# Kernel optimization log

Hardware: AMD Instinct MI355X
Metric: run time of the kernel (lower is better)

The kernel has to match this reference:

```python
import jax, jax.numpy as jnp
import numpy as np

B, N, DIN, DINNER, DOUT, W = 4, 8192, 512, 512, 512, 128


def setup_inputs() -> dict:
    key = jax.random.key(0)
    k1, k2, k3 = jax.random.split(key, 3)
    x = jax.random.normal(k1, (B, N, DIN), jnp.float32)
    # torch Linear weights: (out_features, in_features)
    w_qkv = jax.random.normal(k2, (3 * DINNER, DIN), jnp.float32) * (DIN ** -0.5)
    w_out = jax.random.normal(k3, (DOUT, DINNER), jnp.float32) * (DINNER ** -0.5)
    b_out = jnp.zeros((DOUT,), jnp.float32)
    return {"x": x, "w_qkv": w_qkv, "w_out": w_out, "b_out": b_out}


def reference(x, w_qkv, w_out, b_out):
    b, n, _ = x.shape
    w = W
    scale = DINNER ** -0.5
    pad = (-n) % w  # pad_to_multiple along seq dim (static)
    xp = jnp.pad(x, ((0, 0), (0, pad), (0, 0)))
    qkv = jnp.einsum('bnd,ed->bne', xp, w_qkv)  # to_qkv, no bias
    q, k, v = jnp.split(qkv, 3, axis=-1)
    win = lambda t: t.reshape(b, -1, w, DINNER)  # b (w n) d -> b w n d
    q, k, v = win(q), win(k), win(v)
    # prepend one zero bucket to k, then overlap prev/current windows.
    kp = jnp.pad(k, ((0, 0), (1, 0), (0, 0), (0, 0)))
    k2 = jnp.concatenate((kp[:, :-1], kp[:, 1:]), axis=2)  # (b, nb, 2w, d)
    # NOTE: source bug replicated — v is also built from k, not v.
    v2 = jnp.concatenate((kp[:, :-1], kp[:, 1:]), axis=2)
    sim = jnp.einsum('bwid,bwjd->bwij', q, k2) * scale  # (b, nb, w, 2w)
    i, j = w, 2 * w
    mask = jnp.triu(jnp.ones((i, j), bool), j - i + 1)
    sim = jnp.where(mask, -jnp.finfo(sim.dtype).max, sim)
    attn = jax.nn.softmax(sim, axis=-1)
    out = jnp.einsum('bwij,bwjd->bwid', attn, v2)
    out = out.reshape(b, -1, DINNER)[:, :n]
    return jnp.einsum('bnd,od->bno', out, w_out) + b_out
```

## Files before the change

kernel.cpp:

```cpp
#include <hip/hip_runtime.h>
#include <cstdint>
#include <cstddef>

typedef float f32x4 __attribute__((ext_vector_type(4)));
typedef short s16x8 __attribute__((ext_vector_type(8)));
typedef short s16x4 __attribute__((ext_vector_type(4)));

#define MFMA_BF16(a, b, c) __builtin_amdgcn_mfma_f32_16x16x32_bf16((a), (b), (c), 0, 0, 0)

#define GLD16(g, l)                                                            \
  __builtin_amdgcn_global_load_lds(                                            \
      (const __attribute__((address_space(1))) void*)(g),                      \
      (__attribute__((address_space(3))) void*)(l), 16, 0, 0)

__device__ __forceinline__ unsigned short f2bf(float f) {
  unsigned int u = __float_as_uint(f);
  u += 0x7FFFu + ((u >> 16) & 1u);
  return (unsigned short)(u >> 16);
}

__device__ __forceinline__ s16x8 cvt8(const float* __restrict__ src) {
  const float4 f0 = *(const float4*)src;
  const float4 f1 = *(const float4*)(src + 4);
  s16x8 h;
  h[0] = (short)f2bf(f0.x); h[1] = (short)f2bf(f0.y);
  h[2] = (short)f2bf(f0.z); h[3] = (short)f2bf(f0.w);
  h[4] = (short)f2bf(f1.x); h[5] = (short)f2bf(f1.y);
  h[6] = (short)f2bf(f1.z); h[7] = (short)f2bf(f1.w);
  return h;
}

#define XN 16777216
#define WQN 524288
#define WON 262144
__global__ __launch_bounds__(256)
void cvt_bf16(const float* __restrict__ x, const float* __restrict__ wqkv,
              const float* __restrict__ wout, unsigned short* __restrict__ xb,
              unsigned short* __restrict__ wb, unsigned short* __restrict__ wob) {
  const size_t i = (size_t)(blockIdx.x * 256 + threadIdx.x) * 8;
  const float* src;
  unsigned short* dst;
  if (i < XN) { src = x + i; dst = xb + i; }
  else if (i < XN + WQN) { src = wqkv + (i - XN); dst = wb + (i - XN); }
  else { src = wout + (i - XN - WQN); dst = wob + (i - XN - WQN); }
  *(s16x8*)dst = cvt8(src);
}

__global__ __launch_bounds__(256)
void gemm_qk(const unsigned short* __restrict__ xb, const unsigned short* __restrict__ wb,
             unsigned short* __restrict__ Q, unsigned short* __restrict__ K) {
  __shared__ unsigned short As[128 * 64];
  __shared__ unsigned short Bs[128 * 64];
  const int t = threadIdx.x;
  const int lane = t & 63, wid = t >> 6;
  const int wm = wid >> 1, wn = wid & 1;
  const int nl = lane & 15, quad = lane >> 4;
  const int m0 = blockIdx.y * 128, n0 = blockIdx.x * 128;
  const int sub = lane >> 3;
  const int lblk = (lane & 7) ^ sub;

  const f32x4 zero = {0.f, 0.f, 0.f, 0.f};
  f32x4 acc[4][4];
#pragma unroll
  for (int i = 0; i < 4; ++i)
#pragma unroll
    for (int j = 0; j < 4; ++j) acc[i][j] = zero;

  const unsigned short* gA = xb + (size_t)(m0 + wid * 32 + sub) * 512 + lblk * 8;
  const unsigned short* gB = wb + (size_t)(n0 + wid * 32 + sub) * 512 + lblk * 8;

  for (int kc = 0; kc < 512; kc += 64) {
#pragma unroll
    for (int ii = 0; ii < 4; ++ii) {
      GLD16(gA + kc + (size_t)(ii * 8) * 512, &As[(wid * 32 + ii * 8) * 64]);
      GLD16(gB + kc + (size_t)(ii * 8) * 512, &Bs[(wid * 32 + ii * 8) * 64]);
    }
    __syncthreads();
#pragma unroll
    for (int ks = 0; ks < 2; ++ks) {
      s16x8 af[4], bf[4];
#pragma unroll
      for (int i = 0; i < 4; ++i)
        af[i] = *(const s16x8*)&As[(wm * 64 + i * 16 + nl) * 64 +
                                   (((ks * 4 + quad) ^ (nl & 7)) * 8)];
#pragma unroll
      for (int j = 0; j < 4; ++j)
        bf[j] = *(const s16x8*)&Bs[(wn * 64 + j * 16 + nl) * 64 +
                                   (((ks * 4 + quad) ^ (nl & 7)) * 8)];
#pragma unroll
      for (int i = 0; i < 4; ++i)
#pragma unroll
        for (int j = 0; j < 4; ++j) acc[i][j] = MFMA_BF16(af[i], bf[j], acc[i][j]);
    }
    __syncthreads();
  }
#pragma unroll
  for (int i = 0; i < 4; ++i) {
    const int mrow = m0 + wm * 64 + i * 16 + quad * 4;
#pragma unroll
    for (int j = 0; j < 4; ++j) {
      const int n = n0 + wn * 64 + j * 16 + nl;
      unsigned short* dst = (n < 512 ? Q : K) + (size_t)mrow * 512 + (n & 511);
#pragma unroll
      for (int r = 0; r < 4; ++r) dst[(size_t)r * 512] = f2bf(acc[i][j][r]);
    }
  }
}

__global__ __launch_bounds__(256)
void gemm_kwt(const unsigned short* __restrict__ K, const unsigned short* __restrict__ wob,
              unsigned short* __restrict__ KWT) {
  __shared__ unsigned short As[128 * 64];
  __shared__ unsigned short Bs[128 * 64];
  const int t = threadIdx.x;
  const int lane = t & 63, wid = t >> 6;
  const int wm = wid >> 1, wn = wid & 1;
  const int nl = lane & 15, quad = lane >> 4;
  const int m0 = blockIdx.y * 128, n0 = blockIdx.x * 128;
  const int sub = lane >> 3, lblk = (lane & 7) ^ sub;

  const f32x4 zero = {0.f, 0.f, 0.f, 0.f};
  f32x4 acc[4][4];
#pragma unroll
  for (int i = 0; i < 4; ++i)
#pragma unroll
    for (int j = 0; j < 4; ++j) acc[i][j] = zero;

  const unsigned short* gA = K + (size_t)(m0 + wid * 32 + sub) * 512 + lblk * 8;
  const unsigned short* gB = wob + (size_t)(n0 + wid * 32 + sub) * 512 + lblk * 8;

  for (int kc = 0; kc < 512; kc += 64) {
#pragma unroll
    for (int ii = 0; ii < 4; ++ii) {
      GLD16(gA + kc + (size_t)(ii * 8) * 512, &As[(wid * 32 + ii * 8) * 64]);
      GLD16(gB + kc + (size_t)(ii * 8) * 512, &Bs[(wid * 32 + ii * 8) * 64]);
    }
    __syncthreads();
#pragma unroll
    for (int ks = 0; ks < 2; ++ks) {
      s16x8 af[4], bf[4];
#pragma unroll
      for (int i = 0; i < 4; ++i)
        af[i] = *(const s16x8*)&As[(wm * 64 + i * 16 + nl) * 64 +
                                   (((ks * 4 + quad) ^ (nl & 7)) * 8)];
#pragma unroll
      for (int j = 0; j < 4; ++j)
        bf[j] = *(const s16x8*)&Bs[(wn * 64 + j * 16 + nl) * 64 +
                                   (((ks * 4 + quad) ^ (nl & 7)) * 8)];
#pragma unroll
      for (int i = 0; i < 4; ++i)
#pragma unroll
        for (int j = 0; j < 4; ++j) acc[i][j] = MFMA_BF16(af[i], bf[j], acc[i][j]);
    }
    __syncthreads();
  }
#pragma unroll
  for (int i = 0; i < 4; ++i) {
    const int m = m0 + wm * 64 + i * 16 + quad * 4;
    const int b = m >> 13, ns = m & 8191;
#pragma unroll
    for (int j = 0; j < 4; ++j) {
      const int o = n0 + wn * 64 + j * 16 + nl;
      s16x4 h;
#pragma unroll
      for (int r = 0; r < 4; ++r) h[r] = (short)f2bf(acc[i][j][r]);
      *(s16x4*)&KWT[(size_t)(b * 512 + o) * 8192 + ns] = h;
    }
  }
}

__global__ __launch_bounds__(512)
void attn_p(const unsigned short* __restrict__ Q, const unsigned short* __restrict__ K,
            unsigned short* __restrict__ P) {
  __shared__ unsigned short Qs[128 * 64];
  __shared__ unsigned short Ks[256 * 64];
  __shared__ float redm[128 * 4];
  __shared__ float reds[128 * 4];
  const int t = threadIdx.x;
  const int bx = blockIdx.x, b = bx >> 6, w = bx & 63;
  const int lane = t & 63, wid = t >> 6;
  const int wm = wid >> 2, wn = wid & 3;
  const int nl = lane & 15, quad = lane >> 4;
  const int sub = lane >> 3, lblk = (lane & 7) ^ sub;

  const f32x4 zero = {0.f, 0.f, 0.f, 0.f};
  f32x4 acc[4][4];
#pragma unroll
  for (int i = 0; i < 4; ++i)
#pragma unroll
    for (int j = 0; j < 4; ++j) acc[i][j] = zero;

  const unsigned short* Qb = Q + (size_t)(b * 8192 + w * 128) * 512;
  const unsigned short* Kb = K + (size_t)(b * 8192) * 512;

  for (int kc = 0; kc < 512; kc += 64) {
#pragma unroll
    for (int ii = 0; ii < 2; ++ii)
      GLD16(Qb + (size_t)(wid * 16 + ii * 8 + sub) * 512 + kc + lblk * 8,
            &Qs[(wid * 16 + ii * 8) * 64]);
#pragma unroll
    for (int ii = 0; ii < 4; ++ii) {
      int sq = w * 128 - 128 + wid * 32 + ii * 8 + sub;
      if (sq < 0) sq = 0;
      GLD16(Kb + (size_t)sq * 512 + kc + lblk * 8, &Ks[(wid * 32 + ii * 8) * 64]);
    }
    __syncthreads();
#pragma unroll
    for (int ks = 0; ks < 2; ++ks) {
      s16x8 af[4], bf[4];
#pragma unroll
      for (int i = 0; i < 4; ++i)
        af[i] = *(const s16x8*)&Qs[(wm * 64 + i * 16 + nl) * 64 +
                                   (((ks * 4 + quad) ^ (nl & 7)) * 8)];
#pragma unroll
      for (int j = 0; j < 4; ++j)
        bf[j] = *(const s16x8*)&Ks[(wn * 64 + j * 16 + nl) * 64 +
                                   (((ks * 4 + quad) ^ (nl & 7)) * 8)];
#pragma unroll
      for (int i = 0; i < 4; ++i)
#pragma unroll
        for (int j = 0; j < 4; ++j) acc[i][j] = MFMA_BF16(af[i], bf[j], acc[i][j]);
    }
    __syncthreads();
  }

  const float scale = 0.04419417382415922f;
  float rmax[4][4];
#pragma unroll
  for (int i = 0; i < 4; ++i) {
#pragma unroll
    for (int r = 0; r < 4; ++r) {
      const int row = wm * 64 + i * 16 + quad * 4 + r;
      float mx = -3.4e38f;
#pragma unroll
      for (int j = 0; j < 4; ++j) {
        const int col = wn * 64 + j * 16 + nl;
        float v = acc[i][j][r] * scale;
        if (col >= 128 && col - 128 > row) v = -3.0e38f;
        if (w == 0 && col < 128) v = 0.0f;
        acc[i][j][r] = v;
        mx = fmaxf(mx, v);
      }
      rmax[i][r] = mx;
    }
  }
#pragma unroll
  for (int off = 1; off < 16; off <<= 1)
#pragma unroll
    for (int i = 0; i < 4; ++i)
#pragma unroll
      for (int r = 0; r < 4; ++r)
        rmax[i][r] = fmaxf(rmax[i][r], __shfl_xor(rmax[i][r], off, 64));
  if (nl == 0) {
#pragma unroll
    for (int i = 0; i < 4; ++i)
#pragma unroll
      for (int r = 0; r < 4; ++r)
        redm[(wm * 64 + i * 16 + quad * 4 + r) * 4 + wn] = rmax[i][r];
  }
  __syncthreads();
  float rsum[4][4];
#pragma unroll
  for (int i = 0; i < 4; ++i) {
#pragma unroll
    for (int r = 0; r < 4; ++r) {
      const f32x4 mv = *(const f32x4*)&redm[(wm * 64 + i * 16 + quad * 4 + r) * 4];
      const float m = fmaxf(fmaxf(mv[0], mv[1]), fmaxf(mv[2], mv[3]));
      float s = 0.f;
#pragma unroll
      for (int j = 0; j < 4; ++j) {
        const float p = __expf(acc[i][j][r] - m);
        acc[i][j][r] = p;
        s += p;
      }
      rsum[i][r] = s;
    }
  }
#pragma unroll
  for (int off = 1; off < 16; off <<= 1)
#pragma unroll
    for (int i = 0; i < 4; ++i)
#pragma unroll
      for (int r = 0; r < 4; ++r) rsum[i][r] += __shfl_xor(rsum[i][r], off, 64);
  if (nl == 0) {
#pragma unroll
    for (int i = 0; i < 4; ++i)
#pragma unroll
      for (int r = 0; r < 4; ++r)
        reds[(wm * 64 + i * 16 + quad * 4 + r) * 4 + wn] = rsum[i][r];
  }
  __syncthreads();
#pragma unroll
  for (int i = 0; i < 4; ++i) {
#pragma unroll
    for (int r = 0; r < 4; ++r) {
      const int row = wm * 64 + i * 16 + quad * 4 + r;
      const f32x4 sv = *(const f32x4*)&reds[row * 4];
      const float inv = 1.0f / (sv[0] + sv[1] + sv[2] + sv[3]);
#pragma unroll
      for (int j = 0; j < 4; ++j) {
        const int col = wn * 64 + j * 16 + nl;
        float pv = acc[i][j][r] * inv;
        if (w == 0 && col < 128) pv = 0.0f;
        P[(size_t)bx * 32768 + (size_t)row * 256 + col] = f2bf(pv);
      }
    }
  }
}

__global__ __launch_bounds__(512)
void gemm_out(const unsigned short* __restrict__ P, const unsigned short* __restrict__ KWT,
              const float* __restrict__ bias, float* __restrict__ out) {
  __shared__ unsigned short As[128 * 64];
  __shared__ unsigned short Bs[256 * 64];
  const int t = threadIdx.x;
  const int wbx = blockIdx.y, b = wbx >> 6, w = wbx & 63;
  const int o0 = blockIdx.x * 256;
  const int lane = t & 63, wid = t >> 6;
  const int wm = wid >> 2, wn = wid & 3;
  const int nl = lane & 15, quad = lane >> 4;
  const int sub = lane >> 3, lblk = (lane & 7) ^ sub;

  const f32x4 zero = {0.f, 0.f, 0.f, 0.f};
  f32x4 acc[4][4];
#pragma unroll
  for (int i = 0; i < 4; ++i)
#pragma unroll
    for (int j = 0; j < 4; ++j) acc[i][j] = zero;

  const unsigned short* Pw = P + (size_t)wbx * 32768;
  const int seqbase = w * 128 - 128;

  for (int kc = 0; kc < 256; kc += 64) {
#pragma unroll
    for (int ii = 0; ii < 2; ++ii)
      GLD16(Pw + (size_t)(wid * 16 + ii * 8 + sub) * 256 + kc + lblk * 8,
            &As[(wid * 16 + ii * 8) * 64]);
    int sq = seqbase + kc + lblk * 8;
    if (sq < 0) sq = 0;
#pragma unroll
    for (int ii = 0; ii < 4; ++ii)
      GLD16(KWT + (size_t)(b * 512 + o0 + wid * 32 + ii * 8 + sub) * 8192 + sq,
            &Bs[(wid * 32 + ii * 8) * 64]);
    __syncthreads();
#pragma unroll
    for (int ks = 0; ks < 2; ++ks) {
      s16x8 af[4], bf[4];
#pragma unroll
      for (int i = 0; i < 4; ++i)
        af[i] = *(const s16x8*)&As[(wm * 64 + i * 16 + nl) * 64 +
                                   (((ks * 4 + quad) ^ (nl & 7)) * 8)];
#pragma unroll
      for (int j = 0; j < 4; ++j)
        bf[j] = *(const s16x8*)&Bs[(wn * 64 + j * 16 + nl) * 64 +
                                   (((ks * 4 + quad) ^ (nl & 7)) * 8)];
#pragma unroll
      for (int i = 0; i < 4; ++i)
#pragma unroll
        for (int j = 0; j < 4; ++j) acc[i][j] = MFMA_BF16(af[i], bf[j], acc[i][j]);
    }
    __syncthreads();
  }
#pragma unroll
  for (int i = 0; i < 4; ++i) {
    const int row = wm * 64 + i * 16 + quad * 4;
#pragma unroll
    for (int j = 0; j < 4; ++j) {
      const int o = o0 + wn * 64 + j * 16 + nl;
      const float bo = bias[o];
      float* dst = out + (size_t)(b * 8192 + w * 128 + row) * 512 + o;
#pragma unroll
      for (int r = 0; r < 4; ++r) dst[(size_t)r * 512] = acc[i][j][r] + bo;
    }
  }
}

extern "C" void kernel_launch(void* const* d_in, const int* in_sizes, int n_in,
                              void* d_out, int out_size, void* d_ws, size_t ws_size,
                              hipStream_t stream) {
  const float* x = (const float*)d_in[0];
  const float* w_qkv = (const float*)d_in[1];
  const float* w_out = (const float*)d_in[2];
  const float* b_out = (const float*)d_in[3];
  float* out = (float*)d_out;

  char* ws = (char*)d_ws;
  unsigned short* Q = (unsigned short*)ws;
  unsigned short* K = (unsigned short*)(ws + (size_t)33554432);
  unsigned short* xb = (unsigned short*)(ws + (size_t)67108864);
  unsigned short* KWT = (unsigned short*)(ws + (size_t)67108864);
  unsigned short* P = (unsigned short*)(ws + (size_t)100663296);
  unsigned short* wb = (unsigned short*)(ws + (size_t)100663296);
  unsigned short* wob = (unsigned short*)(ws + (size_t)100663296 + 1048576);

  cvt_bf16<<<dim3(8576), dim3(256), 0, stream>>>(x, w_qkv, w_out, xb, wb, wob);
  gemm_qk<<<dim3(8, 256), dim3(256), 0, stream>>>(xb, wb, Q, K);
  gemm_kwt<<<dim3(4, 256), dim3(256), 0, stream>>>(K, wob, KWT);
  attn_p<<<dim3(256), dim3(512), 0, stream>>>(Q, K, P);
  gemm_out<<<dim3(2, 256), dim3(512), 0, stream>>>(P, KWT, b_out, out);
}
```

Before: 262.4 us.

## Fuse attention probabilities with output GEMM and remap blocks for XCD locality

Merges the attention-probability kernel and the output GEMM into one kernel that keeps the probability tile in swizzled shared memory, so the P buffer no longer goes through global memory. Attention blocks are split into 64-query halves with 256 threads, which doubles the block count. The GEMM kernels now use a 1D grid with an XCD-aware tile mapping. gemm_qk swaps operands so it can write Q/K with vectorized 4-element stores. The fused kernel reloads KWT tiles per output chunk, and each block recomputes the window's QK^T for only half the rows, which adds more K reloads per query.

```diff
diff --git a/kernel.cpp b/kernel.cpp
--- a/kernel.cpp
+++ b/kernel.cpp
@@ -32,7 +32,6 @@
 
 #define XN 16777216
 #define WQN 524288
-#define WON 262144
 __global__ __launch_bounds__(256)
 void cvt_bf16(const float* __restrict__ x, const float* __restrict__ wqkv,
               const float* __restrict__ wout, unsigned short* __restrict__ xb,
@@ -51,13 +50,14 @@
              unsigned short* __restrict__ Q, unsigned short* __restrict__ K) {
   __shared__ unsigned short As[128 * 64];
   __shared__ unsigned short Bs[128 * 64];
-  const int t = threadIdx.x;
-  const int lane = t & 63, wid = t >> 6;
+  const int t = threadIdx.x, lane = t & 63, wid = t >> 6;
   const int wm = wid >> 1, wn = wid & 1;
   const int nl = lane & 15, quad = lane >> 4;
-  const int m0 = blockIdx.y * 128, n0 = blockIdx.x * 128;
-  const int sub = lane >> 3;
-  const int lblk = (lane & 7) ^ sub;
+  const int sub = lane >> 3, lblk = (lane & 7) ^ sub;
+  const int l = blockIdx.x;
+  const int xcd = l & 7, g = l >> 3;
+  const int mt = (g >> 3) * 8 + xcd, nt = g & 7;
+  const int m0 = mt * 128, n0 = nt * 128;
 
   const f32x4 zero = {0.f, 0.f, 0.f, 0.f};
   f32x4 acc[4][4];
@@ -66,14 +66,14 @@
 #pragma unroll
     for (int j = 0; j < 4; ++j) acc[i][j] = zero;
 
-  const unsigned short* gA = xb + (size_t)(m0 + wid * 32 + sub) * 512 + lblk * 8;
-  const unsigned short* gB = wb + (size_t)(n0 + wid * 32 + sub) * 512 + lblk * 8;
+  const unsigned short* gX = xb + (size_t)(m0 + wid * 32 + sub) * 512 + lblk * 8;
+  const unsigned short* gW = wb + (size_t)(n0 + wid * 32 + sub) * 512 + lblk * 8;
 
   for (int kc = 0; kc < 512; kc += 64) {
 #pragma unroll
     for (int ii = 0; ii < 4; ++ii) {
-      GLD16(gA + kc + (size_t)(ii * 8) * 512, &As[(wid * 32 + ii * 8) * 64]);
-      GLD16(gB + kc + (size_t)(ii * 8) * 512, &Bs[(wid * 32 + ii * 8) * 64]);
+      GLD16(gW + kc + (size_t)(ii * 8) * 512, &As[(wid * 32 + ii * 8) * 64]);
+      GLD16(gX + kc + (size_t)(ii * 8) * 512, &Bs[(wid * 32 + ii * 8) * 64]);
     }
     __syncthreads();
 #pragma unroll
@@ -96,13 +96,16 @@
   }
 #pragma unroll
   for (int i = 0; i < 4; ++i) {
-    const int mrow = m0 + wm * 64 + i * 16 + quad * 4;
+    const int n = n0 + wm * 64 + i * 16 + quad * 4;
+    unsigned short* base = (n < 512 ? Q : K);
+    const int nn = n & 511;
 #pragma unroll
     for (int j = 0; j < 4; ++j) {
-      const int n = n0 + wn * 64 + j * 16 + nl;
-      unsigned short* dst = (n < 512 ? Q : K) + (size_t)mrow * 512 + (n & 511);
-#pragma unroll
-      for (int r = 0; r < 4; ++r) dst[(size_t)r * 512] = f2bf(acc[i][j][r]);
+      const int m = m0 + wn * 64 + j * 16 + nl;
+      s16x4 h;
+#pragma unroll
+      for (int r = 0; r < 4; ++r) h[r] = (short)f2bf(acc[i][j][r]);
+      *(s16x4*)&base[(size_t)m * 512 + nn] = h;
     }
   }
 }
@@ -112,12 +115,14 @@
               unsigned short* __restrict__ KWT) {
   __shared__ unsigned short As[128 * 64];
   __shared__ unsigned short Bs[128 * 64];
-  const int t = threadIdx.x;
-  const int lane = t & 63, wid = t >> 6;
+  const int t = threadIdx.x, lane = t & 63, wid = t >> 6;
   const int wm = wid >> 1, wn = wid & 1;
   const int nl = lane & 15, quad = lane >> 4;
-  const int m0 = blockIdx.y * 128, n0 = blockIdx.x * 128;
   const int sub = lane >> 3, lblk = (lane & 7) ^ sub;
+  const int l = blockIdx.x;
+  const int xcd = l & 7, g = l >> 3;
+  const int mt = (g >> 2) * 8 + xcd, nt = g & 3;
+  const int m0 = mt * 128, n0 = nt * 128;
 
   const f32x4 zero = {0.f, 0.f, 0.f, 0.f};
   f32x4 acc[4][4];
@@ -156,8 +161,8 @@
   }
 #pragma unroll
   for (int i = 0; i < 4; ++i) {
-    const int m = m0 + wm * 64 + i * 16 + quad * 4;
-    const int b = m >> 13, ns = m & 8191;
+    const int ms = m0 + wm * 64 + i * 16 + quad * 4;
+    const int b = ms >> 13, ns = ms & 8191;
 #pragma unroll
     for (int j = 0; j < 4; ++j) {
       const int o = n0 + wn * 64 + j * 16 + nl;
@@ -169,19 +174,24 @@
   }
 }
 
-__global__ __launch_bounds__(512)
-void attn_p(const unsigned short* __restrict__ Q, const unsigned short* __restrict__ K,
-            unsigned short* __restrict__ P) {
-  __shared__ unsigned short Qs[128 * 64];
-  __shared__ unsigned short Ks[256 * 64];
-  __shared__ float redm[128 * 4];
-  __shared__ float reds[128 * 4];
-  const int t = threadIdx.x;
-  const int bx = blockIdx.x, b = bx >> 6, w = bx & 63;
-  const int lane = t & 63, wid = t >> 6;
-  const int wm = wid >> 2, wn = wid & 3;
+__global__ __launch_bounds__(256)
+void attn64(const unsigned short* __restrict__ Q, const unsigned short* __restrict__ K,
+            const unsigned short* __restrict__ KWT, const float* __restrict__ bias,
+            float* __restrict__ out) {
+  __shared__ char smem[49152];
+  unsigned short* Qs = (unsigned short*)smem;
+  unsigned short* Ks = (unsigned short*)(smem + 8192);
+  unsigned short* Ps = (unsigned short*)smem;
+  unsigned short* Bs2 = (unsigned short*)(smem + 32768);
+  __shared__ float redm[256];
+  __shared__ float reds[256];
+  const int t = threadIdx.x, lane = t & 63, wid = t >> 6;
+  const int wn = wid;
   const int nl = lane & 15, quad = lane >> 4;
   const int sub = lane >> 3, lblk = (lane & 7) ^ sub;
+  const int bx = blockIdx.x;
+  const int xcd = bx & 7, half = (bx >> 3) & 1, g = bx >> 4;
+  const int wb = g * 8 + xcd, b = wb >> 6, w = wb & 63;
 
   const f32x4 zero = {0.f, 0.f, 0.f, 0.f};
   f32x4 acc[4][4];
@@ -190,7 +200,7 @@
 #pragma unroll
     for (int j = 0; j < 4; ++j) acc[i][j] = zero;
 
-  const unsigned short* Qb = Q + (size_t)(b * 8192 + w * 128) * 512;
+  const unsigned short* Qb = Q + (size_t)(b * 8192 + w * 128 + half * 64) * 512;
   const unsigned short* Kb = K + (size_t)(b * 8192) * 512;
 
   for (int kc = 0; kc < 512; kc += 64) {
@@ -199,10 +209,10 @@
       GLD16(Qb + (size_t)(wid * 16 + ii * 8 + sub) * 512 + kc + lblk * 8,
             &Qs[(wid * 16 + ii * 8) * 64]);
 #pragma unroll
-    for (int ii = 0; ii < 4; ++ii) {
-      int sq = w * 128 - 128 + wid * 32 + ii * 8 + sub;
+    for (int ii = 0; ii < 8; ++ii) {
+      int sq = w * 128 - 128 + wid * 64 + ii * 8 + sub;
       if (sq < 0) sq = 0;
-      GLD16(Kb + (size_t)sq * 512 + kc + lblk * 8, &Ks[(wid * 32 + ii * 8) * 64]);
+      GLD16(Kb + (size_t)sq * 512 + kc + lblk * 8, &Ks[(wid * 64 + ii * 8) * 64]);
     }
     __syncthreads();
 #pragma unroll
@@ -210,7 +220,7 @@
       s16x8 af[4], bf[4];
 #pragma unroll
       for (int i = 0; i < 4; ++i)
-        af[i] = *(const s16x8*)&Qs[(wm * 64 + i * 16 + nl) * 64 +
+        af[i] = *(const s16x8*)&Qs[(i * 16 + nl) * 64 +
                                    (((ks * 4 + quad) ^ (nl & 7)) * 8)];
 #pragma unroll
       for (int j = 0; j < 4; ++j)
@@ -230,13 +240,13 @@
   for (int i = 0; i < 4; ++i) {
 #pragma unroll
     for (int r = 0; r < 4; ++r) {
-      const int row = wm * 64 + i * 16 + quad * 4 + r;
+      const int qrow = half * 64 + i * 16 + quad * 4 + r;
       float mx = -3.4e38f;
 #pragma unroll
       for (int j = 0; j < 4; ++j) {
         const int col = wn * 64 + j * 16 + nl;
         float v = acc[i][j][r] * scale;
-        if (col >= 128 && col - 128 > row) v = -3.0e38f;
+        if (col >= 128 && col - 128 > qrow) v = -3.0e38f;
         if (w == 0 && col < 128) v = 0.0f;
         acc[i][j][r] = v;
         mx = fmaxf(mx, v);
@@ -256,7 +266,7 @@
     for (int i = 0; i < 4; ++i)
 #pragma unroll
       for (int r = 0; r < 4; ++r)
-        redm[(wm * 64 + i * 16 + quad * 4 + r) * 4 + wn] = rmax[i][r];
+        redm[(i * 16 + quad * 4 + r) * 4 + wn] = rmax[i][r];
   }
   __syncthreads();
   float rsum[4][4];
@@ -264,7 +274,7 @@
   for (int i = 0; i < 4; ++i) {
 #pragma unroll
     for (int r = 0; r < 4; ++r) {
-      const f32x4 mv = *(const f32x4*)&redm[(wm * 64 + i * 16 + quad * 4 + r) * 4];
+      const f32x4 mv = *(const f32x4*)&redm[(i * 16 + quad * 4 + r) * 4];
       const float m = fmaxf(fmaxf(mv[0], mv[1]), fmaxf(mv[2], mv[3]));
       float s = 0.f;
 #pragma unroll
@@ -287,14 +297,14 @@
     for (int i = 0; i < 4; ++i)
 #pragma unroll
       for (int r = 0; r < 4; ++r)
-        reds[(wm * 64 + i * 16 + quad * 4 + r) * 4 + wn] = rsum[i][r];
+        reds[(i * 16 + quad * 4 + r) * 4 + wn] = rsum[i][r];
   }
   __syncthreads();
 #pragma unroll
   for (int i = 0; i < 4; ++i) {
 #pragma unroll
     for (int r = 0; r < 4; ++r) {
-      const int row = wm * 64 + i * 16 + quad * 4 + r;
+      const int row = i * 16 + quad * 4 + r;
       const f32x4 sv = *(const f32x4*)&reds[row * 4];
       const float inv = 1.0f / (sv[0] + sv[1] + sv[2] + sv[3]);
 #pragma unroll
@@ -302,75 +312,60 @@
         const int col = wn * 64 + j * 16 + nl;
         float pv = acc[i][j][r] * inv;
         if (w == 0 && col < 128) pv = 0.0f;
-        P[(size_t)bx * 32768 + (size_t)row * 256 + col] = f2bf(pv);
-      }
-    }
-  }
-}
-
-__global__ __launch_bounds__(512)
-void gemm_out(const unsigned short* __restrict__ P, const unsigned short* __restrict__ KWT,
-              const float* __restrict__ bias, float* __restrict__ out) {
-  __shared__ unsigned short As[128 * 64];
-  __shared__ unsigned short Bs[256 * 64];
-  const int t = threadIdx.x;
-  const int wbx = blockIdx.y, b = wbx >> 6, w = wbx & 63;
-  const int o0 = blockIdx.x * 256;
-  const int lane = t & 63, wid = t >> 6;
-  const int wm = wid >> 2, wn = wid & 3;
-  const int nl = lane & 15, quad = lane >> 4;
-  const int sub = lane >> 3, lblk = (lane & 7) ^ sub;
-
-  const f32x4 zero = {0.f, 0.f, 0.f, 0.f};
-  f32x4 acc[4][4];
-#pragma unroll
-  for (int i = 0; i < 4; ++i)
-#pragma unroll
-    for (int j = 0; j < 4; ++j) acc[i][j] = zero;
-
-  const unsigned short* Pw = P + (size_t)wbx * 32768;
+        const int cb = col >> 3;
+        Ps[row * 256 + (((cb ^ (row & 7)) << 3) | (col & 7))] = f2bf(pv);
+      }
+    }
+  }
+  __syncthreads();
+
   const int seqbase = w * 128 - 128;
-
-  for (int kc = 0; kc < 256; kc += 64) {
-#pragma unroll
-    for (int ii = 0; ii < 2; ++ii)
-      GLD16(Pw + (size_t)(wid * 16 + ii * 8 + sub) * 256 + kc + lblk * 8,
-            &As[(wid * 16 + ii * 8) * 64]);
-    int sq = seqbase + kc + lblk * 8;
-    if (sq < 0) sq = 0;
-#pragma unroll
-    for (int ii = 0; ii < 4; ++ii)
-      GLD16(KWT + (size_t)(b * 512 + o0 + wid * 32 + ii * 8 + sub) * 8192 + sq,
-            &Bs[(wid * 32 + ii * 8) * 64]);
-    __syncthreads();
-#pragma unroll
-    for (int ks = 0; ks < 2; ++ks) {
-      s16x8 af[4], bf[4];
-#pragma unroll
-      for (int i = 0; i < 4; ++i)
-        af[i] = *(const s16x8*)&As[(wm * 64 + i * 16 + nl) * 64 +
-                                   (((ks * 4 + quad) ^ (nl & 7)) * 8)];
-#pragma unroll
-      for (int j = 0; j < 4; ++j)
-        bf[j] = *(const s16x8*)&Bs[(wn * 64 + j * 16 + nl) * 64 +
-                                   (((ks * 4 + quad) ^ (nl & 7)) * 8)];
-#pragma unroll
-      for (int i = 0; i < 4; ++i)
-#pragma unroll
-        for (int j = 0; j < 4; ++j) acc[i][j] = MFMA_BF16(af[i], bf[j], acc[i][j]);
-    }
-    __syncthreads();
-  }
-#pragma unroll
-  for (int i = 0; i < 4; ++i) {
-    const int row = wm * 64 + i * 16 + quad * 4;
-#pragma unroll
-    for (int j = 0; j < 4; ++j) {
-      const int o = o0 + wn * 64 + j * 16 + nl;
-      const float bo = bias[o];
-      float* dst = out + (size_t)(b * 8192 + w * 128 + row) * 512 + o;
-#pragma unroll
-      for (int r = 0; r < 4; ++r) dst[(size_t)r * 512] = acc[i][j][r] + bo;
+#pragma unroll 1
+  for (int och = 0; och < 4; ++och) {
+    f32x4 acc2[4][2];
+#pragma unroll
+    for (int i = 0; i < 4; ++i)
+#pragma unroll
+      for (int j = 0; j < 2; ++j) acc2[i][j] = zero;
+#pragma unroll 1
+    for (int kch = 0; kch < 4; ++kch) {
+      int sq = seqbase + kch * 64 + lblk * 8;
+      if (sq < 0) sq = 0;
+#pragma unroll
+      for (int ii = 0; ii < 4; ++ii) {
+        const int orow = och * 128 + wid * 32 + ii * 8 + sub;
+        GLD16(KWT + (size_t)(b * 512 + orow) * 8192 + sq, &Bs2[(wid * 32 + ii * 8) * 64]);
+      }
+      __syncthreads();
+#pragma unroll
+      for (int ks = 0; ks < 2; ++ks) {
+        const int kb = kch * 8 + ks * 4 + quad;
+        s16x8 af[4], bf[2];
+#pragma unroll
+        for (int i = 0; i < 4; ++i)
+          af[i] = *(const s16x8*)&Ps[(i * 16 + nl) * 256 + ((kb ^ (nl & 7)) << 3)];
+#pragma unroll
+        for (int j = 0; j < 2; ++j)
+          bf[j] = *(const s16x8*)&Bs2[(wn * 32 + j * 16 + nl) * 64 +
+                                      (((ks * 4 + quad) ^ (nl & 7)) * 8)];
+#pragma unroll
+        for (int i = 0; i < 4; ++i)
+#pragma unroll
+          for (int j = 0; j < 2; ++j) acc2[i][j] = MFMA_BF16(af[i], bf[j], acc2[i][j]);
+      }
+      __syncthreads();
+    }
+#pragma unroll
+    for (int i = 0; i < 4; ++i) {
+      const int seq = w * 128 + half * 64 + i * 16 + quad * 4;
+      float* dst = out + (size_t)(b * 8192 + seq) * 512;
+#pragma unroll
+      for (int j = 0; j < 2; ++j) {
+        const int o = och * 128 + wn * 32 + j * 16 + nl;
+        const float bo = bias[o];
+#pragma unroll
+        for (int r = 0; r < 4; ++r) dst[(size_t)r * 512 + o] = acc2[i][j][r] + bo;
+      }
     }
   }
 }
@@ -389,13 +384,11 @@
   unsigned short* K = (unsigned short*)(ws + (size_t)33554432);
   unsigned short* xb = (unsigned short*)(ws + (size_t)67108864);
   unsigned short* KWT = (unsigned short*)(ws + (size_t)67108864);
-  unsigned short* P = (unsigned short*)(ws + (size_t)100663296);
   unsigned short* wb = (unsigned short*)(ws + (size_t)100663296);
   unsigned short* wob = (unsigned short*)(ws + (size_t)100663296 + 1048576);
 
   cvt_bf16<<<dim3(8576), dim3(256), 0, stream>>>(x, w_qkv, w_out, xb, wb, wob);
-  gemm_qk<<<dim3(8, 256), dim3(256), 0, stream>>>(xb, wb, Q, K);
-  gemm_kwt<<<dim3(4, 256), dim3(256), 0, stream>>>(K, wob, KWT);
-  attn_p<<<dim3(256), dim3(512), 0, stream>>>(Q, K, P);
-  gemm_out<<<dim3(2, 256), dim3(512), 0, stream>>>(P, KWT, b_out, out);
-}
+  gemm_qk<<<dim3(2048), dim3(256), 0, stream>>>(xb, wb, Q, K);
+  gemm_kwt<<<dim3(1024), dim3(256), 0, stream>>>(K, wob, KWT);
+  attn64<<<dim3(512), dim3(256), 0, stream>>>(Q, K, KWT, b_out, out);
+}
```

Result: faster. 238.7 us (-9.0%).
